# Kernel optimization log

Hardware: AMD Instinct MI355X
Metric: run time of the kernel (lower is better)

Reference implementation:

```python
import jax, jax.numpy as jnp
import numpy as np

N = 100000
E = 1600000
D_IN = 128
D_H = 128


def setup_inputs() -> dict:
    key = jax.random.key(0)
    ks = jax.random.split(key, 10)
    x = jax.random.normal(ks[0], (N, D_IN), dtype=jnp.float32)
    src = jax.random.randint(ks[1], (E,), 0, N)
    dst = jax.random.randint(ks[2], (E,), 0, N)
    s1 = 1.0 / np.sqrt(D_IN)
    s2 = 1.0 / np.sqrt(D_H)
    W_self1 = jax.random.uniform(ks[3], (D_H, D_IN), jnp.float32, -s1, s1)
    W_neigh1 = jax.random.uniform(ks[4], (D_H, D_IN), jnp.float32, -s1, s1)
    b1 = jnp.zeros((D_H,), jnp.float32)
    W_self2 = jax.random.uniform(ks[5], (D_H, D_H), jnp.float32, -s2, s2)
    W_neigh2 = jax.random.uniform(ks[6], (D_H, D_H), jnp.float32, -s2, s2)
    b2 = jnp.zeros((D_H,), jnp.float32)
    return {"x": x, "src": src, "dst": dst,
            "W_self1": W_self1, "W_neigh1": W_neigh1, "b1": b1,
            "W_self2": W_self2, "W_neigh2": W_neigh2, "b2": b2}


def _sage_conv(h, src, dst, W_self, W_neigh, b):
    n = h.shape[0]
    msg = h[src]  # [E, d] gather of source node features
    agg = jax.ops.segment_sum(msg, dst, num_segments=n)  # [N, d]
    deg = jax.ops.segment_sum(jnp.ones((src.shape[0],), h.dtype), dst, num_segments=n)
    h_neigh = agg / jnp.maximum(deg, 1.0)[:, None]  # mean; isolated nodes -> 0
    return h @ W_self.T + h_neigh @ W_neigh.T + b


def reference(x, src, dst, W_self1, W_neigh1, b1, W_self2, W_neigh2, b2):
    h = _sage_conv(x, src, dst, W_self1, W_neigh1, b1)
    h = jax.nn.relu(h)
    h = _sage_conv(h, src, dst, W_self2, W_neigh2, b2)
    return h
```

## Files before the change

### kernel.cpp

```cpp
#include <hip/hip_runtime.h>


typedef unsigned int uint;
typedef unsigned short ushort;
typedef unsigned char uchar;
using short8 = __attribute__((ext_vector_type(8))) short;
using f32x4  = __attribute__((ext_vector_type(4))) float;

__device__ __forceinline__ float bflo(uint u) { return __uint_as_float(u << 16); }
__device__ __forceinline__ float bfhi(uint u) { return __uint_as_float(u & 0xffff0000u); }
__device__ __forceinline__ ushort f2bf(float f) {
  uint u = __float_as_uint(f);
  return (ushort)((u + 0x7fffu + ((u >> 16) & 1u)) >> 16);
}

#define EPB 4096
#define NBKT_MAX 512
#define SLAB_CAP 5120


__global__ __launch_bounds__(256) void x_to_frag_kernel(
    const float* __restrict__ x, ushort* __restrict__ xf, int n) {
  const int tile = blockIdx.x;
  const int s = threadIdx.x >> 6;
  const int l = threadIdx.x & 63;
  const int row = tile * 16 + (l & 15);
  const int k = s * 32 + (l >> 4) * 8;
  ushort4 r0 = {0, 0, 0, 0}, r1 = {0, 0, 0, 0};
  if (row < n) {
    const float* p = x + (size_t)row * 128 + k;
    float4 a = ((const float4*)p)[0];
    float4 b = ((const float4*)p)[1];
    r0.x = f2bf(a.x); r0.y = f2bf(a.y); r0.z = f2bf(a.z); r0.w = f2bf(a.w);
    r1.x = f2bf(b.x); r1.y = f2bf(b.y); r1.z = f2bf(b.z); r1.w = f2bf(b.w);
  }
  ushort* dp = xf + (size_t)tile * 2048 + s * 512 + l * 8;
  *(ushort4*)dp = r0;
  *(ushort4*)(dp + 4) = r1;
}

__global__ __launch_bounds__(256) void w_to_frag_kernel(
    const float* __restrict__ w0, const float* __restrict__ w1,
    const float* __restrict__ w2, const float* __restrict__ w3,
    ushort* __restrict__ o0, ushort* __restrict__ o1,
    ushort* __restrict__ o2, ushort* __restrict__ o3) {
  const float* in = (blockIdx.y == 0) ? w0 : (blockIdx.y == 1) ? w1
                    : (blockIdx.y == 2) ? w2 : w3;
  ushort* out = (blockIdx.y == 0) ? o0 : (blockIdx.y == 1) ? o1
                : (blockIdx.y == 2) ? o2 : o3;
  const int tile = blockIdx.x;
  const int s = threadIdx.x >> 6;
  const int l = threadIdx.x & 63;
  const int row = tile * 16 + (l & 15);
  const int k = s * 32 + (l >> 4) * 8;
  const float* p = in + (size_t)row * 128 + k;
  float4 a = ((const float4*)p)[0];
  float4 b = ((const float4*)p)[1];
  ushort4 r0, r1;
  r0.x = f2bf(a.x); r0.y = f2bf(a.y); r0.z = f2bf(a.z); r0.w = f2bf(a.w);
  r1.x = f2bf(b.x); r1.y = f2bf(b.y); r1.z = f2bf(b.z); r1.w = f2bf(b.w);
  ushort* dp = out + (size_t)tile * 2048 + s * 512 + l * 8;
  *(ushort4*)dp = r0;
  *(ushort4*)(dp + 4) = r1;
}

template <int IN_F32>
__global__ __launch_bounds__(256) void quant_rows_kernel(
    const void* __restrict__ in_, uchar* __restrict__ outq,
    float* __restrict__ scales, int n) {
  int node = (blockIdx.x * 256 + threadIdx.x) >> 5;
  int lane = threadIdx.x & 31;
  if (node >= n) return;
  float f[4];
  if (IN_F32) {
    float4 v = *(const float4*)((const float*)in_ + (size_t)node * 128 + lane * 4);
    f[0] = v.x; f[1] = v.y; f[2] = v.z; f[3] = v.w;
  } else {
    const ushort* hp = (const ushort*)in_ + (size_t)(node >> 4) * 2048 +
                       (lane >> 3) * 512 +
                       (((lane >> 1) & 3) * 16 + (node & 15)) * 8 +
                       (lane & 1) * 4;
    uint2 v = *(const uint2*)hp;
    f[0] = bflo(v.x); f[1] = bfhi(v.x); f[2] = bflo(v.y); f[3] = bfhi(v.y);
  }
  float mx = fmaxf(fmaxf(fabsf(f[0]), fabsf(f[1])),
                   fmaxf(fabsf(f[2]), fabsf(f[3])));
#pragma unroll
  for (int off = 1; off < 32; off <<= 1) mx = fmaxf(mx, __shfl_xor(mx, off, 64));
  float inv = (mx > 0.f) ? 127.0f / mx : 0.f;
  uint q0 = (uint)(__float2int_rn(f[0] * inv) + 128);
  uint q1 = (uint)(__float2int_rn(f[1] * inv) + 128);
  uint q2 = (uint)(__float2int_rn(f[2] * inv) + 128);
  uint q3 = (uint)(__float2int_rn(f[3] * inv) + 128);
  uint packed = q0 | (q1 << 8) | (q2 << 16) | (q3 << 24);
  *(uint*)(outq + (size_t)node * 128 + lane * 4) = packed;
  if (lane == 0) scales[node] = (mx > 0.f) ? mx / 127.0f : 0.f;
}

__global__ __launch_bounds__(256) void partition_kernel(
    const int* __restrict__ src, const int* __restrict__ dst,
    int* __restrict__ bktcnt, uint* __restrict__ gpart, int E, int nbkt) {
  __shared__ uint staged[EPB];
  __shared__ ushort stagedb[EPB];
  __shared__ int hist[NBKT_MAX];
  __shared__ int scanex[NBKT_MAX];
  __shared__ int lcur[NBKT_MAX];
  __shared__ int gbase[NBKT_MAX];
  __shared__ int s2[256];
  const int t = threadIdx.x;
  const int e0 = blockIdx.x * EPB;
  const int total = min(EPB, E - e0);

  hist[t] = 0; hist[t + 256] = 0;
  __syncthreads();

  int myb[16];
  uint myu[16];
#pragma unroll
  for (int q = 0; q < 16; ++q) {
    int e = e0 + q * 256 + t;
    if (e < E) {
      int s = src[e], d = dst[e];
      myb[q] = d >> 8;
      myu[q] = (uint)s | ((uint)(d & 255) << 24);
      atomicAdd(&hist[myb[q]], 1);
    } else {
      myb[q] = -1;
      myu[q] = 0;
    }
  }
  __syncthreads();

  int h0 = hist[2 * t], h1 = hist[2 * t + 1];
  s2[t] = h0 + h1;
  __syncthreads();
  for (int off = 1; off < 256; off <<= 1) {
    int v = (t >= off) ? s2[t - off] : 0;
    __syncthreads();
    s2[t] += v;
    __syncthreads();
  }
  int ex2 = s2[t] - (h0 + h1);
  scanex[2 * t] = ex2;
  scanex[2 * t + 1] = ex2 + h0;
  lcur[2 * t] = ex2;
  lcur[2 * t + 1] = ex2 + h0;
  __syncthreads();

#pragma unroll
  for (int q = 0; q < 2; ++q) {
    int b = t + q * 256;
    int c = hist[b];
    gbase[b] = (b < nbkt && c > 0)
                   ? (b * SLAB_CAP + atomicAdd(&bktcnt[b], c))
                   : 0;
  }

#pragma unroll
  for (int q = 0; q < 16; ++q) {
    if (myb[q] >= 0) {
      int p = atomicAdd(&lcur[myb[q]], 1);
      staged[p] = myu[q];
      stagedb[p] = (ushort)myb[q];
    }
  }
  __syncthreads();

  for (int i = t; i < total; i += 256) {
    int b = stagedb[i];
    gpart[gbase[b] + (i - scanex[b])] = staged[i];
  }
}

__global__ __launch_bounds__(512) void bucket_scan_kernel(
    const int* __restrict__ bktcnt, int* __restrict__ bucket_base,
    int* __restrict__ row_start, int nbkt, int n, int E) {
  __shared__ int sh[512];
  int t = threadIdx.x;
  int v = (t < nbkt) ? bktcnt[t] : 0;
  sh[t] = v;
  __syncthreads();
  for (int off = 1; off < 512; off <<= 1) {
    int u = (t >= off) ? sh[t - off] : 0;
    __syncthreads();
    sh[t] += u;
    __syncthreads();
  }
  if (t < nbkt) bucket_base[t] = sh[t] - v;
  if (t == 0) row_start[n] = E;
}

__global__ __launch_bounds__(256) void fine_fill_kernel(
    const uint* __restrict__ gpart, const int* __restrict__ bktcnt,
    const int* __restrict__ bucket_base, int* __restrict__ row_start,
    int* __restrict__ csr, int n) {
  __shared__ int hist[256];
  __shared__ int pfx[256];
  __shared__ int lcur[256];
  const int b = blockIdx.x;
  const int t = threadIdx.x;
  const int cnt = bktcnt[b];
  const uint* sl = gpart + (size_t)b * SLAB_CAP;
  hist[t] = 0;
  __syncthreads();
  for (int i = t; i < cnt; i += 256) atomicAdd(&hist[sl[i] >> 24], 1);
  __syncthreads();
  int h = hist[t];
  pfx[t] = h;
  __syncthreads();
  for (int off = 1; off < 256; off <<= 1) {
    int u = (t >= off) ? pfx[t - off] : 0;
    __syncthreads();
    pfx[t] += u;
    __syncthreads();
  }
  const int base = bucket_base[b] + pfx[t] - h;
  const int n0 = b << 8;
  if (n0 + t < n) row_start[n0 + t] = base;
  lcur[t] = base;
  __syncthreads();
  for (int i = t; i < cnt; i += 256) {
    uint u = sl[i];
    int p = atomicAdd(&lcur[u >> 24], 1);
    csr[p] = (int)(u & 0xFFFFFFu);
  }
}

__global__ __launch_bounds__(256) void aggregate_mean_i8_kernel(
    const uchar* __restrict__ hq, const float* __restrict__ scales,
    const int* __restrict__ csr, const int* __restrict__ row_start,
    ushort* __restrict__ outf, int n) {
  int node = (blockIdx.x * 256 + threadIdx.x) >> 5;
  int lane = threadIdx.x & 31;
  if (node >= n) return;
  const int sub = lane >> 4;
  const int dlo = (lane & 15) * 8;
  int e0 = row_start[node], e1 = row_start[node + 1];
  float a0 = 0.f, a1 = 0.f, a2 = 0.f, a3 = 0.f;
  float a4 = 0.f, a5 = 0.f, a6 = 0.f, a7 = 0.f;
  if (e1 > e0) {
    const int elast = e1 - 1;
    float csum = 0.f;
    for (int j0 = e0; j0 < e1; j0 += 8) {
      uint2 v[4];
      float sm[4];
#pragma unroll
      for (int q = 0; q < 4; ++q) {
        int j = j0 + 2 * q + sub;
        int jc = (j <= elast) ? j : elast;
        int s = csr[jc];
        v[q] = *(const uint2*)(hq + (size_t)s * 128 + dlo);
        float m = (j <= elast) ? 1.0f : 0.0f;
        sm[q] = m * scales[s];
      }
#pragma unroll
      for (int q = 0; q < 4; ++q) {
        const uint lo = v[q].x, hi = v[q].y;
        const float s_ = sm[q];
        a0 = fmaf((float)(lo & 255), s_, a0);
        a1 = fmaf((float)((lo >> 8) & 255), s_, a1);
        a2 = fmaf((float)((lo >> 16) & 255), s_, a2);
        a3 = fmaf((float)(lo >> 24), s_, a3);
        a4 = fmaf((float)(hi & 255), s_, a4);
        a5 = fmaf((float)((hi >> 8) & 255), s_, a5);
        a6 = fmaf((float)((hi >> 16) & 255), s_, a6);
        a7 = fmaf((float)(hi >> 24), s_, a7);
        csum += s_;
      }
    }
    const float c128 = 128.0f * csum;
    a0 -= c128; a1 -= c128; a2 -= c128; a3 -= c128;
    a4 -= c128; a5 -= c128; a6 -= c128; a7 -= c128;
    a0 += __shfl_xor(a0, 16, 64);
    a1 += __shfl_xor(a1, 16, 64);
    a2 += __shfl_xor(a2, 16, 64);
    a3 += __shfl_xor(a3, 16, 64);
    a4 += __shfl_xor(a4, 16, 64);
    a5 += __shfl_xor(a5, 16, 64);
    a6 += __shfl_xor(a6, 16, 64);
    a7 += __shfl_xor(a7, 16, 64);
    float inv = 1.0f / (float)(e1 - e0);
    a0 *= inv; a1 *= inv; a2 *= inv; a3 *= inv;
    a4 *= inv; a5 *= inv; a6 *= inv; a7 *= inv;
  }
  if (lane < 16) {
    uint4 r;
    r.x = (uint)f2bf(a0) | ((uint)f2bf(a1) << 16);
    r.y = (uint)f2bf(a2) | ((uint)f2bf(a3) << 16);
    r.z = (uint)f2bf(a4) | ((uint)f2bf(a5) << 16);
    r.w = (uint)f2bf(a6) | ((uint)f2bf(a7) << 16);
    ushort* dp = outf + (size_t)(node >> 4) * 2048 + (lane >> 2) * 512 +
                 ((lane & 3) * 16 + (node & 15)) * 8;
    *(uint4*)dp = r;
  }
}

template <int RELU, int OUT_FRAG>
__global__ __launch_bounds__(256, 4) void sage_gemm_mfma_kernel(
    const ushort* __restrict__ hs, const ushort* __restrict__ hn,
    const ushort* __restrict__ Wsf, const ushort* __restrict__ Wnf,
    const float* __restrict__ bias, void* __restrict__ out_, int n) {
  const int w = threadIdx.x >> 6;
  const int lane = threadIdx.x & 63;
  const int lr = lane & 15;
  const int m0 = blockIdx.x * 64;
  if (m0 >= n) return;

  short8 bs[2][4], bn[2][4];
  float bv[2];
#pragma unroll
  for (int u = 0; u < 2; ++u) {
    const int ot = w + u * 4;
    const ushort* qs = Wsf + (size_t)ot * 2048 + lane * 8;
    const ushort* qn = Wnf + (size_t)ot * 2048 + lane * 8;
#pragma unroll
    for (int s = 0; s < 4; ++s) {
      bs[u][s] = *(const short8*)(qs + s * 512);
      bn[u][s] = *(const short8*)(qn + s * 512);
    }
    bv[u] = bias[ot * 16 + lr];
  }

  const int nmt = min(4, (n - m0 + 15) >> 4);
  for (int mt = 0; mt < nmt; ++mt) {
    const int tile = (m0 >> 4) + mt;
    short8 as[4], an[4];
    {
      const ushort* ps = hs + (size_t)tile * 2048 + lane * 8;
      const ushort* pq = hn + (size_t)tile * 2048 + lane * 8;
#pragma unroll
      for (int s = 0; s < 4; ++s) {
        as[s] = *(const short8*)(ps + s * 512);
        an[s] = *(const short8*)(pq + s * 512);
      }
    }
    const int rbase = (lane >> 4) * 4;
    const int mbase = m0 + mt * 16 + rbase;
#pragma unroll
    for (int u = 0; u < 2; ++u) {
      f32x4 acc = {0.f, 0.f, 0.f, 0.f};
#pragma unroll
      for (int s = 0; s < 4; ++s)
        acc = __builtin_amdgcn_mfma_f32_16x16x32_bf16(as[s], bs[u][s], acc, 0, 0, 0);
#pragma unroll
      for (int s = 0; s < 4; ++s)
        acc = __builtin_amdgcn_mfma_f32_16x16x32_bf16(an[s], bn[u][s], acc, 0, 0, 0);
      const int ot = w + u * 4;
      const size_t cu = (size_t)(ot >> 1) * 512 +
                        (((ot & 1) * 2 + (lr >> 3)) * 16) * 8 + (lr & 7);
#pragma unroll
      for (int r = 0; r < 4; ++r) {
        int node = mbase + r;
        if (node < n) {
          float v = acc[r] + bv[u];
          if (RELU) v = fmaxf(v, 0.f);
          if (OUT_FRAG) {
            ((ushort*)out_)[(size_t)tile * 2048 + (rbase + r) * 8 + cu] = f2bf(v);
          } else {
            ((float*)out_)[(size_t)node * 128 + ot * 16 + lr] = v;
          }
        }
      }
    }
  }
}

extern "C" void kernel_launch(void* const* d_in, const int* in_sizes, int n_in,
                              void* d_out, int out_size, void* d_ws, size_t ws_size,
                              hipStream_t stream) {
  const float* x   = (const float*)d_in[0];
  const int*   src = (const int*)d_in[1];
  const int*   dst = (const int*)d_in[2];
  const float* Ws1 = (const float*)d_in[3];
  const float* Wn1 = (const float*)d_in[4];
  const float* b1  = (const float*)d_in[5];
  const float* Ws2 = (const float*)d_in[6];
  const float* Wn2 = (const float*)d_in[7];
  const float* b2  = (const float*)d_in[8];
  float* out = (float*)d_out;
  const int D = 128;
  const int N = in_sizes[0] / D;
  const int E = in_sizes[1];
  (void)n_in; (void)out_size; (void)ws_size;

  const int tiles = (N + 15) >> 4;

  char* p = (char*)d_ws;
  auto carve = [&](size_t bytes) {
    char* r = p;
    p += (bytes + 255) & ~(size_t)255;
    return r;
  };
  int*    bktcnt      = (int*)carve(NBKT_MAX * 4);
  int*    bucket_base = (int*)carve(NBKT_MAX * 4);
  int*    row_start   = (int*)carve((size_t)(N + 1) * 4);
  uint*   gpart       = (uint*)carve((size_t)NBKT_MAX * SLAB_CAP * 4);
  int*    csr         = (int*)carve((size_t)E * 4);
  ushort* xbf         = (ushort*)carve((size_t)tiles * 2048 * 2);
  ushort* h1f         = (ushort*)carve((size_t)tiles * 2048 * 2);
  ushort* hnf         = (ushort*)carve((size_t)tiles * 2048 * 2);
  float*  xs          = (float*)carve((size_t)N * 4);
  float*  h1s         = (float*)carve((size_t)N * 4);
  ushort* Wf1s        = (ushort*)carve((size_t)D * D * 2);
  ushort* Wf1n        = (ushort*)carve((size_t)D * D * 2);
  ushort* Wf2s        = (ushort*)carve((size_t)D * D * 2);
  ushort* Wf2n        = (ushort*)carve((size_t)D * D * 2);
  uchar* xq  = (uchar*)h1f;
  uchar* h1q = (uchar*)xbf;

  hipMemsetAsync(bktcnt, 0, NBKT_MAX * 4, stream);

  const int nbkt = (N + 255) >> 8;

  x_to_frag_kernel<<<tiles, 256, 0, stream>>>(x, xbf, N);
  {
    dim3 g(8, 4);
    w_to_frag_kernel<<<g, 256, 0, stream>>>(Ws1, Wn1, Ws2, Wn2,
                                            Wf1s, Wf1n, Wf2s, Wf2n);
  }
  quant_rows_kernel<1><<<(N + 7) / 8, 256, 0, stream>>>(x, xq, xs, N);

  partition_kernel<<<(E + EPB - 1) / EPB, 256, 0, stream>>>(src, dst, bktcnt, gpart, E, nbkt);
  bucket_scan_kernel<<<1, 512, 0, stream>>>(bktcnt, bucket_base, row_start, nbkt, N, E);
  fine_fill_kernel<<<nbkt, 256, 0, stream>>>(gpart, bktcnt, bucket_base, row_start, csr, N);

  const int gblocks = (N + 63) / 64;

  aggregate_mean_i8_kernel<<<(N + 7) / 8, 256, 0, stream>>>(xq, xs, csr, row_start, hnf, N);
  sage_gemm_mfma_kernel<1, 1><<<gblocks, 256, 0, stream>>>(
      xbf, hnf, Wf1s, Wf1n, b1, h1f, N);

  quant_rows_kernel<0><<<(N + 7) / 8, 256, 0, stream>>>(h1f, h1q, h1s, N);

  aggregate_mean_i8_kernel<<<(N + 7) / 8, 256, 0, stream>>>(h1q, h1s, csr, row_start, hnf, N);
  sage_gemm_mfma_kernel<0, 0><<<gblocks, 256, 0, stream>>>(
      h1f, hnf, Wf2s, Wf2n, b2, out, N);
}
```

Before: 206.2 us.

## Fuse x bf16 fragment conversion with int8 quantization; double-buffer aggregate gathers

The separate x-to-fragment and fp32 quantization kernels are merged into one x_prep kernel. It reads each row of x once and writes both the bf16 MFMA fragment layout and the int8 rows with their scales, which removes a second full pass over the fp32 input and one launch. The int8 mean-aggregation loop is restructured to double-buffer its neighbor gathers, issuing the next group's CSR and row loads before accumulating the current group, so load latency is hidden. The cost is more live registers in the aggregation kernel, which could reduce occupancy.

```diff
diff --git a/kernel.cpp b/kernel.cpp
--- a/kernel.cpp
+++ b/kernel.cpp
@@ -19,24 +19,31 @@
 #define SLAB_CAP 5120
 
 
-__global__ __launch_bounds__(256) void x_to_frag_kernel(
-    const float* __restrict__ x, ushort* __restrict__ xf, int n) {
-  const int tile = blockIdx.x;
-  const int s = threadIdx.x >> 6;
-  const int l = threadIdx.x & 63;
-  const int row = tile * 16 + (l & 15);
-  const int k = s * 32 + (l >> 4) * 8;
-  ushort4 r0 = {0, 0, 0, 0}, r1 = {0, 0, 0, 0};
-  if (row < n) {
-    const float* p = x + (size_t)row * 128 + k;
-    float4 a = ((const float4*)p)[0];
-    float4 b = ((const float4*)p)[1];
-    r0.x = f2bf(a.x); r0.y = f2bf(a.y); r0.z = f2bf(a.z); r0.w = f2bf(a.w);
-    r1.x = f2bf(b.x); r1.y = f2bf(b.y); r1.z = f2bf(b.z); r1.w = f2bf(b.w);
-  }
-  ushort* dp = xf + (size_t)tile * 2048 + s * 512 + l * 8;
-  *(ushort4*)dp = r0;
-  *(ushort4*)(dp + 4) = r1;
+__global__ __launch_bounds__(256) void x_prep_kernel(
+    const float* __restrict__ x, ushort* __restrict__ xf,
+    uchar* __restrict__ outq, float* __restrict__ scales, int n) {
+  int node = (blockIdx.x * 256 + threadIdx.x) >> 5;
+  int lane = threadIdx.x & 31;
+  if (node >= n) return;
+  float4 v = *(const float4*)(x + (size_t)node * 128 + lane * 4);
+  float f[4] = {v.x, v.y, v.z, v.w};
+  ushort4 r;
+  r.x = f2bf(f[0]); r.y = f2bf(f[1]); r.z = f2bf(f[2]); r.w = f2bf(f[3]);
+  ushort* dp = xf + (size_t)(node >> 4) * 2048 + (lane >> 3) * 512 +
+               (((lane >> 1) & 3) * 16 + (node & 15)) * 8 + (lane & 1) * 4;
+  *(ushort4*)dp = r;
+  float mx = fmaxf(fmaxf(fabsf(f[0]), fabsf(f[1])),
+                   fmaxf(fabsf(f[2]), fabsf(f[3])));
+#pragma unroll
+  for (int off = 1; off < 32; off <<= 1) mx = fmaxf(mx, __shfl_xor(mx, off, 64));
+  float inv = (mx > 0.f) ? 127.0f / mx : 0.f;
+  uint q0 = (uint)(__float2int_rn(f[0] * inv) + 128);
+  uint q1 = (uint)(__float2int_rn(f[1] * inv) + 128);
+  uint q2 = (uint)(__float2int_rn(f[2] * inv) + 128);
+  uint q3 = (uint)(__float2int_rn(f[3] * inv) + 128);
+  *(uint*)(outq + (size_t)node * 128 + lane * 4) =
+      q0 | (q1 << 8) | (q2 << 16) | (q3 << 24);
+  if (lane == 0) scales[node] = (mx > 0.f) ? mx / 127.0f : 0.f;
 }
 
 __global__ __launch_bounds__(256) void w_to_frag_kernel(
@@ -64,25 +71,16 @@
   *(ushort4*)(dp + 4) = r1;
 }
 
-template <int IN_F32>
-__global__ __launch_bounds__(256) void quant_rows_kernel(
-    const void* __restrict__ in_, uchar* __restrict__ outq,
+__global__ __launch_bounds__(256) void quant_frag_kernel(
+    const ushort* __restrict__ in_, uchar* __restrict__ outq,
     float* __restrict__ scales, int n) {
   int node = (blockIdx.x * 256 + threadIdx.x) >> 5;
   int lane = threadIdx.x & 31;
   if (node >= n) return;
-  float f[4];
-  if (IN_F32) {
-    float4 v = *(const float4*)((const float*)in_ + (size_t)node * 128 + lane * 4);
-    f[0] = v.x; f[1] = v.y; f[2] = v.z; f[3] = v.w;
-  } else {
-    const ushort* hp = (const ushort*)in_ + (size_t)(node >> 4) * 2048 +
-                       (lane >> 3) * 512 +
-                       (((lane >> 1) & 3) * 16 + (node & 15)) * 8 +
-                       (lane & 1) * 4;
-    uint2 v = *(const uint2*)hp;
-    f[0] = bflo(v.x); f[1] = bfhi(v.x); f[2] = bflo(v.y); f[3] = bfhi(v.y);
-  }
+  const ushort* hp = in_ + (size_t)(node >> 4) * 2048 + (lane >> 3) * 512 +
+                     (((lane >> 1) & 3) * 16 + (node & 15)) * 8 + (lane & 1) * 4;
+  uint2 v = *(const uint2*)hp;
+  float f[4] = {bflo(v.x), bfhi(v.x), bflo(v.y), bfhi(v.y)};
   float mx = fmaxf(fmaxf(fabsf(f[0]), fabsf(f[1])),
                    fmaxf(fabsf(f[2]), fabsf(f[3])));
 #pragma unroll
@@ -92,8 +90,8 @@
   uint q1 = (uint)(__float2int_rn(f[1] * inv) + 128);
   uint q2 = (uint)(__float2int_rn(f[2] * inv) + 128);
   uint q3 = (uint)(__float2int_rn(f[3] * inv) + 128);
-  uint packed = q0 | (q1 << 8) | (q2 << 16) | (q3 << 24);
-  *(uint*)(outq + (size_t)node * 128 + lane * 4) = packed;
+  *(uint*)(outq + (size_t)node * 128 + lane * 4) =
+      q0 | (q1 << 8) | (q2 << 16) | (q3 << 24);
   if (lane == 0) scales[node] = (mx > 0.f) ? mx / 127.0f : 0.f;
 }
 
@@ -241,33 +239,45 @@
   if (e1 > e0) {
     const int elast = e1 - 1;
     float csum = 0.f;
-    for (int j0 = e0; j0 < e1; j0 += 8) {
-      uint2 v[4];
-      float sm[4];
-#pragma unroll
-      for (int q = 0; q < 4; ++q) {
-        int j = j0 + 2 * q + sub;
-        int jc = (j <= elast) ? j : elast;
-        int s = csr[jc];
-        v[q] = *(const uint2*)(hq + (size_t)s * 128 + dlo);
-        float m = (j <= elast) ? 1.0f : 0.0f;
-        sm[q] = m * scales[s];
-      }
-#pragma unroll
-      for (int q = 0; q < 4; ++q) {
-        const uint lo = v[q].x, hi = v[q].y;
-        const float s_ = sm[q];
-        a0 = fmaf((float)(lo & 255), s_, a0);
-        a1 = fmaf((float)((lo >> 8) & 255), s_, a1);
-        a2 = fmaf((float)((lo >> 16) & 255), s_, a2);
-        a3 = fmaf((float)(lo >> 24), s_, a3);
-        a4 = fmaf((float)(hi & 255), s_, a4);
-        a5 = fmaf((float)((hi >> 8) & 255), s_, a5);
-        a6 = fmaf((float)((hi >> 16) & 255), s_, a6);
-        a7 = fmaf((float)(hi >> 24), s_, a7);
-        csum += s_;
-      }
-    }
+    uint2 vA[4], vB[4];
+    float smA[4], smB[4];
+
+#define LOADG(V, SM, gj0)                                        \
+    _Pragma("unroll") for (int q = 0; q < 4; ++q) {              \
+      int j = (gj0) + 2 * q + sub;                               \
+      int jc = (j <= elast) ? j : elast;                         \
+      int s = csr[jc];                                           \
+      V[q] = *(const uint2*)(hq + (size_t)s * 128 + dlo);        \
+      SM[q] = ((j <= elast) ? 1.0f : 0.0f) * scales[s];          \
+    }
+#define ACCG(V, SM)                                              \
+    _Pragma("unroll") for (int q = 0; q < 4; ++q) {              \
+      const uint lo = V[q].x, hi = V[q].y;                       \
+      const float s_ = SM[q];                                    \
+      a0 = fmaf((float)(lo & 255), s_, a0);                      \
+      a1 = fmaf((float)((lo >> 8) & 255), s_, a1);               \
+      a2 = fmaf((float)((lo >> 16) & 255), s_, a2);              \
+      a3 = fmaf((float)(lo >> 24), s_, a3);                      \
+      a4 = fmaf((float)(hi & 255), s_, a4);                      \
+      a5 = fmaf((float)((hi >> 8) & 255), s_, a5);               \
+      a6 = fmaf((float)((hi >> 16) & 255), s_, a6);              \
+      a7 = fmaf((float)(hi >> 24), s_, a7);                      \
+      csum += s_;                                                \
+    }
+
+    const int G = (e1 - e0 + 7) >> 3;
+    LOADG(vA, smA, e0);
+    int g = 0;
+    for (; g + 2 <= G; g += 2) {
+      LOADG(vB, smB, e0 + (g + 1) * 8);
+      ACCG(vA, smA);
+      if (g + 2 < G) LOADG(vA, smA, e0 + (g + 2) * 8);
+      ACCG(vB, smB);
+    }
+    if (G & 1) ACCG(vA, smA);
+#undef LOADG
+#undef ACCG
+
     const float c128 = 128.0f * csum;
     a0 -= c128; a1 -= c128; a2 -= c128; a3 -= c128;
     a4 -= c128; a5 -= c128; a6 -= c128; a7 -= c128;
@@ -412,13 +422,12 @@
 
   const int nbkt = (N + 255) >> 8;
 
-  x_to_frag_kernel<<<tiles, 256, 0, stream>>>(x, xbf, N);
+  x_prep_kernel<<<(N + 7) / 8, 256, 0, stream>>>(x, xbf, xq, xs, N);
   {
     dim3 g(8, 4);
     w_to_frag_kernel<<<g, 256, 0, stream>>>(Ws1, Wn1, Ws2, Wn2,
                                             Wf1s, Wf1n, Wf2s, Wf2n);
   }
-  quant_rows_kernel<1><<<(N + 7) / 8, 256, 0, stream>>>(x, xq, xs, N);
 
   partition_kernel<<<(E + EPB - 1) / EPB, 256, 0, stream>>>(src, dst, bktcnt, gpart, E, nbkt);
   bucket_scan_kernel<<<1, 512, 0, stream>>>(bktcnt, bucket_base, row_start, nbkt, N, E);
@@ -430,7 +439,7 @@
   sage_gemm_mfma_kernel<1, 1><<<gblocks, 256, 0, stream>>>(
       xbf, hnf, Wf1s, Wf1n, b1, h1f, N);
 
-  quant_rows_kernel<0><<<(N + 7) / 8, 256, 0, stream>>>(h1f, h1q, h1s, N);
+  quant_frag_kernel<<<(N + 7) / 8, 256, 0, stream>>>(h1f, h1q, h1s, N);
 
   aggregate_mean_i8_kernel<<<(N + 7) / 8, 256, 0, stream>>>(h1q, h1s, csr, row_start, hnf, N);
   sage_gemm_mfma_kernel<0, 0><<<gblocks, 256, 0, stream>>>(
```

After: 206.4 us. Within noise of the previous version (+0.1%).
